# Kernel optimization log

Measured on AMD Instinct MI355X. Metric: run time of the kernel, lower is better.

The kernel has to match this reference:

```python
import jax, jax.numpy as jnp
import numpy as np

DIM, HIDDEN, E = 1024, 4096, 8
B, L = 2, 2048


def setup_inputs() -> dict:
    key = jax.random.key(0)
    ks = jax.random.split(key, 6)
    s_in = 1.0 / np.sqrt(DIM)
    s_h = 1.0 / np.sqrt(HIDDEN)
    return {
        "x": jax.random.normal(ks[0], (B, L, DIM), dtype=jnp.float32),
        "Wg": jax.random.uniform(ks[1], (E, DIM), jnp.float32, -s_in, s_in),
        "W1": jax.random.uniform(ks[2], (E, DIM, HIDDEN), jnp.float32, -s_in, s_in),
        "b1": jax.random.uniform(ks[3], (E, HIDDEN), jnp.float32, -s_in, s_in),
        "W2": jax.random.uniform(ks[4], (E, HIDDEN, DIM), jnp.float32, -s_h, s_h),
        "b2": jax.random.uniform(ks[5], (E, DIM), jnp.float32, -s_h, s_h),
    }


def reference(x, Wg, W1, b1, W2, b2):
    # Router: top-1 over gate logits (softmax is monotone, argmax of probs == argmax of logits)
    gate_logits = jnp.einsum("bld,ed->ble", x, Wg)  # [B, L, E]
    top1 = jnp.argmax(gate_logits, axis=-1)          # [B, L] int
    out = jnp.zeros_like(x)
    # Fixed small loop over experts (structurally distinct weights); per-expert
    # dense MLP + select, honoring top-1 dispatch/combine semantics.
    for e in range(E):
        mask = (top1 == e)[..., None]                                   # [B, L, 1]
        h = jax.nn.gelu(jnp.einsum("bld,dh->blh", x, W1[e]) + b1[e],
                        approximate=False)                              # [B, L, H]
        y = jnp.einsum("blh,hd->bld", h, W2[e]) + b2[e]                 # [B, L, D]
        out = jnp.where(mask, y, out)
    return out
```

## Files before the change

kernel.cpp:

```cpp
#include <hip/hip_runtime.h>
#include <hip/hip_bf16.h>
#include <math.h>

#define NTOK 4096
#define DIMSZ 1024
#define HID 4096
#define NE 8
#define RT256 24

typedef unsigned short u16;
typedef unsigned int u32;
typedef __attribute__((ext_vector_type(8))) short bf16x8;
typedef __attribute__((ext_vector_type(4))) float f32x4;

#define AS1 __attribute__((address_space(1)))
#define AS3 __attribute__((address_space(3)))

#define SWZ(r) (((r) >> 1) & 3)

static __device__ __forceinline__ u16 f2bf(float f) {
    u32 u = __float_as_uint(f);
    u32 r = u + 0x7fffu + ((u >> 16) & 1u);
    return (u16)(r >> 16);
}

static __device__ __forceinline__ u32 pk2bf(float lo, float hi) {
    __hip_bfloat162 h = __float22bfloat162_rn(make_float2(lo, hi));
    return *(u32*)&h;
}

__global__ void k_init(int* counts, int* cursor) {
    if (threadIdx.x < NE) { counts[threadIdx.x] = 0; cursor[threadIdx.x] = 0; }
}

__global__ void k_zero(float* p) {
    int i = blockIdx.x * 1024 + threadIdx.x * 4;
    *(float4*)(p + i) = make_float4(0.f, 0.f, 0.f, 0.f);
}

__global__ __launch_bounds__(256) void k_router(const float* __restrict__ x,
                                                const float* __restrict__ Wg,
                                                int* __restrict__ ids,
                                                int* __restrict__ counts) {
    int wave = threadIdx.x >> 6;
    int lane = threadIdx.x & 63;
    int t = blockIdx.x * 4 + wave;

    const float4* xr = (const float4*)(x + (size_t)t * DIMSZ);
    float4 xv[4];
#pragma unroll
    for (int j = 0; j < 4; j++) xv[j] = xr[j * 64 + lane];

    float s[NE];
#pragma unroll
    for (int e = 0; e < NE; e++) {
        const float4* wr = (const float4*)(Wg + (size_t)e * DIMSZ);
        float p = 0.f;
#pragma unroll
        for (int j = 0; j < 4; j++) {
            float4 w = wr[j * 64 + lane];
            p += xv[j].x * w.x + xv[j].y * w.y + xv[j].z * w.z + xv[j].w * w.w;
        }
#pragma unroll
        for (int m = 32; m >= 1; m >>= 1) p += __shfl_xor(p, m, 64);
        s[e] = p;
    }
    if (lane == 0) {
        int best = 0;
#pragma unroll
        for (int e = 1; e < NE; e++) if (s[e] > s[best]) best = e;
        ids[t] = best;
        atomicAdd(&counts[best], 1);
    }
}

__global__ void k_scan(const int* __restrict__ counts, int* __restrict__ offs) {
    if (threadIdx.x == 0) {
        int a = 0;
        for (int e = 0; e < NE; e++) { offs[e] = a; a += counts[e]; }
    }
}

__global__ __launch_bounds__(256) void k_gather(const float* __restrict__ x,
                                                const int* __restrict__ ids,
                                                const int* __restrict__ offs,
                                                int* __restrict__ cursor,
                                                int* __restrict__ perm,
                                                u16* __restrict__ Xg) {
    int t = blockIdx.x;
    __shared__ int sp;
    if (threadIdx.x == 0) {
        int e = ids[t];
        int p = offs[e] + atomicAdd(&cursor[e], 1);
        perm[p] = t;
        sp = p;
    }
    __syncthreads();
    int p = sp;
    float4 v = ((const float4*)(x + (size_t)t * DIMSZ))[threadIdx.x];
    *(uint2*)(Xg + (size_t)p * DIMSZ + threadIdx.x * 4) =
        make_uint2(pk2bf(v.x, v.y), pk2bf(v.z, v.w));
}

__global__ __launch_bounds__(256) void k_wt(const float* __restrict__ W1,
                                            const float* __restrict__ W2,
                                            u16* __restrict__ W1T,
                                            u16* __restrict__ W2T) {
    int bid = blockIdx.x;
    const float* src;
    u16* dst;
    int K, N, kt, nt;
    if (bid < 8192) {
        int e = bid >> 10, t = bid & 1023;
        kt = t >> 6; nt = t & 63;
        src = W1 + (size_t)e * 1024 * 4096;
        dst = W1T + (size_t)e * 4096 * 1024;
        K = 1024; N = 4096;
    } else {
        int b = bid - 8192;
        int e = b >> 10, t = b & 1023;
        kt = t >> 4; nt = t & 15;
        src = W2 + (size_t)e * 4096 * 1024;
        dst = W2T + (size_t)e * 1024 * 4096;
        K = 4096; N = 1024;
    }
    __shared__ u32 T[32][65];
    int tid = threadIdx.x;
#pragma unroll
    for (int pass = 0; pass < 2; pass++) {
        int kp = (tid >> 4) + pass * 16;
        int nc = (tid & 15) * 4;
        const float* r0 = src + (size_t)(kt * 64 + 2 * kp) * N + nt * 64 + nc;
        float4 a = *(const float4*)r0;
        float4 b = *(const float4*)(r0 + N);
        T[kp][nc + 0] = pk2bf(a.x, b.x);
        T[kp][nc + 1] = pk2bf(a.y, b.y);
        T[kp][nc + 2] = pk2bf(a.z, b.z);
        T[kp][nc + 3] = pk2bf(a.w, b.w);
    }
    __syncthreads();
    int n = tid >> 2;
    int sb = (tid & 3) * 8;
    u16* orow = dst + (size_t)(nt * 64 + n) * K + kt * 64;
#pragma unroll
    for (int p = 0; p < 2; p++) {
        int s = sb + p * 4;
        *(uint4*)(orow + 2 * s) = make_uint4(T[s][n], T[s + 1][n], T[s + 2][n], T[s + 3][n]);
    }
}

template <int KDIM, int NDIM, int EPI, int KSPLIT>
__global__ __launch_bounds__(512, 4) void k_gemm(const u16* __restrict__ A,
                                                 const u16* __restrict__ Wt,
                                                 const float* __restrict__ biasAll,
                                                 const int* __restrict__ counts,
                                                 const int* __restrict__ offs,
                                                 const int* __restrict__ perm,
                                                 u16* __restrict__ Hout,
                                                 float* __restrict__ Fout) {
    constexpr int NT = NDIM / 128;
    constexpr int NREST = NT * KSPLIT;
    constexpr int NWG = RT256 * NREST;
    constexpr int CPX = NWG / 8;
    constexpr int KL = KDIM / KSPLIT;
    constexpr int NKL = KL / 32;
    int bid = blockIdx.x;
    int wid = (bid & 7) * CPX + (bid >> 3);
    int x = wid / NREST;
    int rest = wid % NREST;
    int ks = rest % KSPLIT;
    int n0 = (rest / KSPLIT) * 128;
    int kbase = ks * KL;

    int e = -1, lrt = 0, a0 = 0;
#pragma unroll
    for (int i = 0; i < NE; i++) {
        int rt = (counts[i] + 255) >> 8;
        if (e < 0 && x < a0 + rt) { e = i; lrt = x - a0; }
        a0 += rt;
    }
    if (e < 0) return;
    int row0 = offs[e] + lrt * 256;
    int nrows = offs[e] + counts[e] - row0;
    if (nrows > 256) nrows = 256;

    __shared__ alignas(16) u16 Asb[3][256][32];
    __shared__ alignas(16) u16 Bsb[3][128][32];

    int tid = threadIdx.x;
    int lane = tid & 63;
    int wave = tid >> 6;
    int wr = wave >> 1;
    int wc = wave & 1;
    int fr = lane & 15, fc = lane >> 4;

    const u16* srcA[2];
    const u16* srcB;
#pragma unroll
    for (int c = 0; c < 2; c++) {
        int g = c * 512 + tid;
        int r = g >> 2, slot = g & 3;
        int rc = r < nrows ? r : nrows - 1;
        srcA[c] = A + (size_t)(row0 + rc) * KDIM + kbase + (slot ^ SWZ(r)) * 8;
    }
    {
        int r = tid >> 2, slot = tid & 3;
        srcB = Wt + (size_t)e * NDIM * KDIM + (size_t)(n0 + r) * KDIM + kbase + (slot ^ SWZ(r)) * 8;
    }

    f32x4 acc[4][4] = {};

    u16 *A0 = &Asb[0][0][0], *A1 = &Asb[1][0][0], *A2 = &Asb[2][0][0];
    u16 *B0 = &Bsb[0][0][0], *B1 = &Bsb[1][0][0], *B2 = &Bsb[2][0][0];

#define STAGE(AD, BD, KT)                                                       \
    {                                                                           \
        _Pragma("unroll")                                                       \
        for (int c = 0; c < 2; c++) {                                           \
            __builtin_amdgcn_global_load_lds(                                   \
                (const AS1 void*)(srcA[c] + (size_t)(KT) * 32),                 \
                (AS3 void*)((AD) + (c * 512 + wave * 64) * 8), 16, 0, 0);       \
        }                                                                       \
        __builtin_amdgcn_global_load_lds(                                       \
            (const AS1 void*)(srcB + (size_t)(KT) * 32),                        \
            (AS3 void*)((BD) + (wave * 64) * 8), 16, 0, 0);                     \
    }

#define COMPUTE(AP, BP)                                                         \
    {                                                                           \
        bf16x8 af[4], bfr[4];                                                   \
        _Pragma("unroll")                                                       \
        for (int m = 0; m < 4; m++) {                                           \
            int r = wr * 64 + m * 16 + fr;                                      \
            af[m] = *(const bf16x8*)((AP) + r * 32 + (fc ^ SWZ(r)) * 8);        \
        }                                                                       \
        _Pragma("unroll")                                                       \
        for (int n = 0; n < 4; n++) {                                           \
            int N = wc * 64 + n * 16 + fr;                                      \
            bfr[n] = *(const bf16x8*)((BP) + N * 32 + (fc ^ SWZ(N)) * 8);       \
        }                                                                       \
        _Pragma("unroll")                                                       \
        for (int m = 0; m < 4; m++)                                             \
            _Pragma("unroll")                                                   \
            for (int n = 0; n < 4; n++)                                         \
                acc[m][n] = __builtin_amdgcn_mfma_f32_16x16x32_bf16(af[m], bfr[n], acc[m][n], 0, 0, 0); \
    }

#define WAITV(N) asm volatile("s_waitcnt vmcnt(" #N ")" ::: "memory")
#define BAR()    __builtin_amdgcn_s_barrier()
#define SCB()    __builtin_amdgcn_sched_barrier(0)

    STAGE(A0, B0, 0);
    STAGE(A1, B1, 1);

    for (int kk = 0; kk < NKL - 2; kk++) {
        WAITV(3);
        BAR();
        SCB();
        STAGE(A2, B2, kk + 2);
        COMPUTE(A0, B0);
        u16* t;
        t = A0; A0 = A1; A1 = A2; A2 = t;
        t = B0; B0 = B1; B1 = B2; B2 = t;
    }
    WAITV(3);
    BAR();
    SCB();
    COMPUTE(A0, B0);
    WAITV(0);
    BAR();
    SCB();
    COMPUTE(A1, B1);

#undef STAGE
#undef COMPUTE
#undef WAITV
#undef BAR
#undef SCB

    int cb = lane & 15;
    int rq = lane >> 4;
#pragma unroll
    for (int m = 0; m < 4; m++) {
        int rbase = wr * 64 + m * 16 + rq * 4;
#pragma unroll
        for (int n = 0; n < 4; n++) {
            int col = n0 + wc * 64 + n * 16 + cb;
            float bias = (EPI == 2 && ks != 0) ? 0.f : biasAll[(size_t)e * NDIM + col];
#pragma unroll
            for (int j = 0; j < 4; j++) {
                int r = rbase + j;
                if (r < nrows) {
                    float v = acc[m][n][j] + bias;
                    int p = row0 + r;
                    if (EPI == 1) {
                        float g = 0.5f * v * (1.0f + erff(v * 0.70710678118654752f));
                        Hout[(size_t)p * NDIM + col] = f2bf(g);
                    } else {
                        atomicAdd(&Fout[(size_t)perm[p] * NDIM + col], v);
                    }
                }
            }
        }
    }
}

extern "C" void kernel_launch(void* const* d_in, const int* in_sizes, int n_in,
                              void* d_out, int out_size, void* d_ws, size_t ws_size,
                              hipStream_t stream) {
    const float* x  = (const float*)d_in[0];
    const float* Wg = (const float*)d_in[1];
    const float* W1 = (const float*)d_in[2];
    const float* b1 = (const float*)d_in[3];
    const float* W2 = (const float*)d_in[4];
    const float* b2 = (const float*)d_in[5];
    float* out = (float*)d_out;

    char* ws = (char*)d_ws;
    int* ids    = (int*)(ws + 0);
    int* counts = (int*)(ws + 16384);
    int* offs   = (int*)(ws + 16448);
    int* cursor = (int*)(ws + 16512);
    int* perm   = (int*)(ws + 16576);

    u16* Xg   = (u16*)(ws + 65536);
    u16* H    = (u16*)(ws + 65536 + 8388608);
    u16* W1T  = (u16*)(ws + 65536 + 8388608 + 33554432);
    u16* W2T  = (u16*)(ws + 65536 + 8388608 + 33554432 + 67108864);

    k_init<<<dim3(1), dim3(64), 0, stream>>>(counts, cursor);
    k_router<<<dim3(NTOK / 4), dim3(256), 0, stream>>>(x, Wg, ids, counts);
    k_scan<<<dim3(1), dim3(64), 0, stream>>>(counts, offs);
    k_gather<<<dim3(NTOK), dim3(256), 0, stream>>>(x, ids, offs, cursor, perm, Xg);
    k_wt<<<dim3(16384), dim3(256), 0, stream>>>(W1, W2, W1T, W2T);
    k_zero<<<dim3(NTOK * DIMSZ / 1024), dim3(256), 0, stream>>>(out);
    k_gemm<DIMSZ, HID, 1, 1><<<dim3(RT256 * (HID / 128)), dim3(512), 0, stream>>>(
        Xg, W1T, b1, counts, offs, perm, H, (float*)nullptr);
    k_gemm<HID, DIMSZ, 2, 2><<<dim3(RT256 * (DIMSZ / 128) * 2), dim3(512), 0, stream>>>(
        H, W2T, b2, counts, offs, perm, (u16*)nullptr, out);
}
```

Baseline: 370.8 us.

## Shrink grouped GEMM row tiles to 128 and drop the init, scan and zero kernels

```diff
diff --git a/kernel.cpp b/kernel.cpp
--- a/kernel.cpp
+++ b/kernel.cpp
@@ -6,7 +6,7 @@
 #define DIMSZ 1024
 #define HID 4096
 #define NE 8
-#define RT256 24
+#define RT_MAX 40
 
 typedef unsigned short u16;
 typedef unsigned int u32;
@@ -27,15 +27,6 @@
 static __device__ __forceinline__ u32 pk2bf(float lo, float hi) {
     __hip_bfloat162 h = __float22bfloat162_rn(make_float2(lo, hi));
     return *(u32*)&h;
-}
-
-__global__ void k_init(int* counts, int* cursor) {
-    if (threadIdx.x < NE) { counts[threadIdx.x] = 0; cursor[threadIdx.x] = 0; }
-}
-
-__global__ void k_zero(float* p) {
-    int i = blockIdx.x * 1024 + threadIdx.x * 4;
-    *(float4*)(p + i) = make_float4(0.f, 0.f, 0.f, 0.f);
 }
 
 __global__ __launch_bounds__(256) void k_router(const float* __restrict__ x,
@@ -74,16 +65,9 @@
     }
 }
 
-__global__ void k_scan(const int* __restrict__ counts, int* __restrict__ offs) {
-    if (threadIdx.x == 0) {
-        int a = 0;
-        for (int e = 0; e < NE; e++) { offs[e] = a; a += counts[e]; }
-    }
-}
-
 __global__ __launch_bounds__(256) void k_gather(const float* __restrict__ x,
                                                 const int* __restrict__ ids,
-                                                const int* __restrict__ offs,
+                                                const int* __restrict__ counts,
                                                 int* __restrict__ cursor,
                                                 int* __restrict__ perm,
                                                 u16* __restrict__ Xg) {
@@ -91,7 +75,9 @@
     __shared__ int sp;
     if (threadIdx.x == 0) {
         int e = ids[t];
-        int p = offs[e] + atomicAdd(&cursor[e], 1);
+        int off = 0;
+        for (int i = 0; i < e; i++) off += counts[i];
+        int p = off + atomicAdd(&cursor[e], 1);
         perm[p] = t;
         sp = p;
     }
@@ -150,17 +136,16 @@
 }
 
 template <int KDIM, int NDIM, int EPI, int KSPLIT>
-__global__ __launch_bounds__(512, 4) void k_gemm(const u16* __restrict__ A,
+__global__ __launch_bounds__(256, 4) void k_gemm(const u16* __restrict__ A,
                                                  const u16* __restrict__ Wt,
                                                  const float* __restrict__ biasAll,
                                                  const int* __restrict__ counts,
-                                                 const int* __restrict__ offs,
                                                  const int* __restrict__ perm,
                                                  u16* __restrict__ Hout,
                                                  float* __restrict__ Fout) {
     constexpr int NT = NDIM / 128;
     constexpr int NREST = NT * KSPLIT;
-    constexpr int NWG = RT256 * NREST;
+    constexpr int NWG = RT_MAX * NREST;
     constexpr int CPX = NWG / 8;
     constexpr int KL = KDIM / KSPLIT;
     constexpr int NKL = KL / 32;
@@ -172,58 +157,62 @@
     int n0 = (rest / KSPLIT) * 128;
     int kbase = ks * KL;
 
-    int e = -1, lrt = 0, a0 = 0;
+    int e = -1, lrt = 0, a0 = 0, off_e = 0, cum = 0;
 #pragma unroll
     for (int i = 0; i < NE; i++) {
-        int rt = (counts[i] + 255) >> 8;
-        if (e < 0 && x < a0 + rt) { e = i; lrt = x - a0; }
+        int c = counts[i];
+        int rt = (c + 127) >> 7;
+        if (e < 0 && x < a0 + rt) { e = i; lrt = x - a0; off_e = cum; }
         a0 += rt;
+        cum += c;
     }
     if (e < 0) return;
-    int row0 = offs[e] + lrt * 256;
-    int nrows = offs[e] + counts[e] - row0;
-    if (nrows > 256) nrows = 256;
-
-    __shared__ alignas(16) u16 Asb[3][256][32];
+    int row0 = off_e + lrt * 128;
+    int nrows = off_e + counts[e] - row0;
+    if (nrows > 128) nrows = 128;
+
+    __shared__ alignas(16) u16 Asb[2][128][32];
     __shared__ alignas(16) u16 Bsb[3][128][32];
 
     int tid = threadIdx.x;
     int lane = tid & 63;
     int wave = tid >> 6;
-    int wr = wave >> 1;
-    int wc = wave & 1;
-    int fr = lane & 15, fc = lane >> 4;
+    int wr = wave >> 1, wc = wave & 1;
 
     const u16* srcA[2];
-    const u16* srcB;
-#pragma unroll
-    for (int c = 0; c < 2; c++) {
-        int g = c * 512 + tid;
+    const u16* srcB[2];
+#pragma unroll
+    for (int p = 0; p < 2; p++) {
+        int g = p * 256 + tid;
         int r = g >> 2, slot = g & 3;
         int rc = r < nrows ? r : nrows - 1;
-        srcA[c] = A + (size_t)(row0 + rc) * KDIM + kbase + (slot ^ SWZ(r)) * 8;
-    }
-    {
-        int r = tid >> 2, slot = tid & 3;
-        srcB = Wt + (size_t)e * NDIM * KDIM + (size_t)(n0 + r) * KDIM + kbase + (slot ^ SWZ(r)) * 8;
+        int kg = (slot ^ SWZ(r)) * 8;
+        srcA[p] = A + (size_t)(row0 + rc) * KDIM + kbase + kg;
+        srcB[p] = Wt + (size_t)e * NDIM * KDIM + (size_t)(n0 + r) * KDIM + kbase + kg;
     }
 
     f32x4 acc[4][4] = {};
-
-    u16 *A0 = &Asb[0][0][0], *A1 = &Asb[1][0][0], *A2 = &Asb[2][0][0];
+    int fr = lane & 15, fc = lane >> 4;
+
+    u16 *Aa = &Asb[0][0][0], *Ab = &Asb[1][0][0];
     u16 *B0 = &Bsb[0][0][0], *B1 = &Bsb[1][0][0], *B2 = &Bsb[2][0][0];
 
-#define STAGE(AD, BD, KT)                                                       \
-    {                                                                           \
-        _Pragma("unroll")                                                       \
-        for (int c = 0; c < 2; c++) {                                           \
+#define STAGE_A(AD, KT)                                                         \
+    if ((KT) < NKL) {                                                           \
+        _Pragma("unroll")                                                       \
+        for (int p = 0; p < 2; p++)                                             \
             __builtin_amdgcn_global_load_lds(                                   \
-                (const AS1 void*)(srcA[c] + (size_t)(KT) * 32),                 \
-                (AS3 void*)((AD) + (c * 512 + wave * 64) * 8), 16, 0, 0);       \
-        }                                                                       \
-        __builtin_amdgcn_global_load_lds(                                       \
-            (const AS1 void*)(srcB + (size_t)(KT) * 32),                        \
-            (AS3 void*)((BD) + (wave * 64) * 8), 16, 0, 0);                     \
+                (const AS1 void*)(srcA[p] + (size_t)(KT) * 32),                 \
+                (AS3 void*)((AD) + (p * 256 + wave * 64) * 8), 16, 0, 0);       \
+    }
+
+#define STAGE_B(BD, KT)                                                         \
+    if ((KT) < NKL) {                                                           \
+        _Pragma("unroll")                                                       \
+        for (int p = 0; p < 2; p++)                                             \
+            __builtin_amdgcn_global_load_lds(                                   \
+                (const AS1 void*)(srcB[p] + (size_t)(KT) * 32),                 \
+                (AS3 void*)((BD) + (p * 256 + wave * 64) * 8), 16, 0, 0);       \
     }
 
 #define COMPUTE(AP, BP)                                                         \
@@ -250,29 +239,28 @@
 #define BAR()    __builtin_amdgcn_s_barrier()
 #define SCB()    __builtin_amdgcn_sched_barrier(0)
 
-    STAGE(A0, B0, 0);
-    STAGE(A1, B1, 1);
-
-    for (int kk = 0; kk < NKL - 2; kk++) {
-        WAITV(3);
+    STAGE_B(B0, 0);
+    STAGE_A(Aa, 0);
+    STAGE_B(B1, 1);
+
+    for (int kk = 0; kk < NKL - 1; kk++) {
+        WAITV(2);
         BAR();
         SCB();
-        STAGE(A2, B2, kk + 2);
-        COMPUTE(A0, B0);
+        STAGE_A(Ab, kk + 1);
+        STAGE_B(B2, kk + 2);
+        COMPUTE(Aa, B0);
         u16* t;
-        t = A0; A0 = A1; A1 = A2; A2 = t;
+        t = Aa; Aa = Ab; Ab = t;
         t = B0; B0 = B1; B1 = B2; B2 = t;
     }
-    WAITV(3);
-    BAR();
-    SCB();
-    COMPUTE(A0, B0);
     WAITV(0);
     BAR();
     SCB();
-    COMPUTE(A1, B1);
-
-#undef STAGE
+    COMPUTE(Aa, B0);
+
+#undef STAGE_A
+#undef STAGE_B
 #undef COMPUTE
 #undef WAITV
 #undef BAR
@@ -319,7 +307,6 @@
     char* ws = (char*)d_ws;
     int* ids    = (int*)(ws + 0);
     int* counts = (int*)(ws + 16384);
-    int* offs   = (int*)(ws + 16448);
     int* cursor = (int*)(ws + 16512);
     int* perm   = (int*)(ws + 16576);
 
@@ -328,14 +315,13 @@
     u16* W1T  = (u16*)(ws + 65536 + 8388608 + 33554432);
     u16* W2T  = (u16*)(ws + 65536 + 8388608 + 33554432 + 67108864);
 
-    k_init<<<dim3(1), dim3(64), 0, stream>>>(counts, cursor);
+    hipMemsetAsync(ws + 16384, 0, 192, stream);
+    hipMemsetAsync(out, 0, (size_t)NTOK * DIMSZ * 4, stream);
     k_router<<<dim3(NTOK / 4), dim3(256), 0, stream>>>(x, Wg, ids, counts);
-    k_scan<<<dim3(1), dim3(64), 0, stream>>>(counts, offs);
-    k_gather<<<dim3(NTOK), dim3(256), 0, stream>>>(x, ids, offs, cursor, perm, Xg);
+    k_gather<<<dim3(NTOK), dim3(256), 0, stream>>>(x, ids, counts, cursor, perm, Xg);
     k_wt<<<dim3(16384), dim3(256), 0, stream>>>(W1, W2, W1T, W2T);
-    k_zero<<<dim3(NTOK * DIMSZ / 1024), dim3(256), 0, stream>>>(out);
-    k_gemm<DIMSZ, HID, 1, 1><<<dim3(RT256 * (HID / 128)), dim3(512), 0, stream>>>(
-        Xg, W1T, b1, counts, offs, perm, H, (float*)nullptr);
-    k_gemm<HID, DIMSZ, 2, 2><<<dim3(RT256 * (DIMSZ / 128) * 2), dim3(512), 0, stream>>>(
-        H, W2T, b2, counts, offs, perm, (u16*)nullptr, out);
-}
+    k_gemm<DIMSZ, HID, 1, 1><<<dim3(RT_MAX * (HID / 128)), dim3(256), 0, stream>>>(
+        Xg, W1T, b1, counts, perm, H, (float*)nullptr);
+    k_gemm<HID, DIMSZ, 2, 4><<<dim3(RT_MAX * (DIMSZ / 128) * 4), dim3(256), 0, stream>>>(
+        H, W2T, b2, counts, perm, (u16*)nullptr, out);
+}
```

After: 415.9 us. 1.12x slower.
